# Performance work log

Measured on AMD Instinct MI355X. Metric: run time of the kernel, lower is better.

The kernel has to match this reference:

```python
import jax, jax.numpy as jnp
import numpy as np

N = 50000          # num nodes (adj_dim)
D = 128            # feature dim
E = 1_600_000      # num edges
C = 1.0            # curvature c_in
NUM_GCN_LAYERS = 3 # num_layers - 1
MIN_NORM = 1e-15
EPS = 1e-5


def hyp_logmap0(x, c):
    # Hyperboloid (Lorentz) logmap at origin, per HGCF manifold code.
    sqrtK = 1.0 / jnp.sqrt(c)            # sqrt(K), K = 1/c
    y = x[..., 1:]                        # spatial part [N, D-1]
    y_norm = jnp.maximum(jnp.linalg.norm(y, axis=-1, keepdims=True), MIN_NORM)
    theta = jnp.maximum(x[..., 0:1] / sqrtK, 1.0 + EPS)
    tail = sqrtK * jnp.arccosh(theta) * y / y_norm
    return jnp.concatenate([jnp.zeros_like(x[..., 0:1]), tail], axis=-1)


def hyp_expmap0(u, c):
    sqrtK = 1.0 / jnp.sqrt(c)
    v = u[..., 1:]
    v_norm = jnp.maximum(jnp.linalg.norm(v, axis=-1, keepdims=True), MIN_NORM)
    theta = v_norm / sqrtK
    first = sqrtK * jnp.cosh(theta)
    tail = sqrtK * jnp.sinh(theta) * v / v_norm
    return jnp.concatenate([first, tail], axis=-1)


def hyp_proj(x, c):
    # Project onto hyperboloid: reset time-like coord from spatial norm.
    K = 1.0 / c
    y = x[..., 1:]
    y_sqnorm = jnp.sum(y * y, axis=-1, keepdims=True)
    first = jnp.sqrt(jnp.maximum(K + y_sqnorm, EPS))
    return jnp.concatenate([first, y], axis=-1)


def spmm(rows, cols, vals, h):
    # sparse [N,N] @ dense [N,D] via gather + segment_sum
    return jax.ops.segment_sum(vals[:, None] * h[cols], rows, num_segments=N)


def setup_inputs() -> dict:
    key = jax.random.key(0)
    k1, k2, k3, k4 = jax.random.split(key, 4)
    # Build valid hyperboloid points: tangent vector at origin (time coord 0),
    # then expmap0 + proj.
    u_tail = 0.1 * jax.random.normal(k1, (N, D - 1), dtype=jnp.float32)
    u = jnp.concatenate([jnp.zeros((N, 1), jnp.float32), u_tail], axis=-1)
    x = hyp_proj(hyp_expmap0(u, C), C)
    adj_rows = jax.random.randint(k2, (E,), 0, N, dtype=jnp.int32)
    adj_cols = jax.random.randint(k3, (E,), 0, N, dtype=jnp.int32)
    # roughly degree-normalized positive edge weights
    adj_vals = jax.random.uniform(k4, (E,), dtype=jnp.float32) / 32.0
    return {"x": x, "adj_rows": adj_rows, "adj_cols": adj_cols, "adj_vals": adj_vals}


def reference(x, adj_rows, adj_cols, adj_vals):
    # HypAgg.forward with network='plainGCN'
    h = hyp_logmap0(x, C)
    for _ in range(NUM_GCN_LAYERS):
        h = spmm(adj_rows, adj_cols, adj_vals, h)
    out = hyp_proj(hyp_expmap0(h, C), C)
    # HyperbolicGraphConvolution returns (h, adj); adj passes through unchanged,
    # so the tensor output is `out`.
    return out
```

## Files before the change

### kernel.cpp

```cpp
#include <hip/hip_runtime.h>
#include <math.h>

#define N_NODES 50000
#define D 128
#define MIN_NORM 1e-15f
#define EPS 1e-5f
#define NBUCK 196
#define CHUNK 4096
#define CAP 9216
#define FSCALE 32.0f
#define INV_FSCALE (1.0f / 32.0f)

typedef float fx2 __attribute__((ext_vector_type(2)));

__global__ __launch_bounds__(256) void binA_kernel(const int* __restrict__ rows,
                                                   const int* __restrict__ cols,
                                                   const float* __restrict__ vals,
                                                   int* __restrict__ gcur,
                                                   int2* __restrict__ tmp, int E) {
    __shared__ int lh[NBUCK];
    __shared__ int lb[NBUCK];
    for (int i = threadIdx.x; i < NBUCK; i += 256) lh[i] = 0;
    __syncthreads();
    int start = blockIdx.x * CHUNK;
    int end = min(start + CHUNK, E);
    for (int i = start + threadIdx.x; i < end; i += 256)
        atomicAdd(&lh[rows[i] >> 8], 1);
    __syncthreads();
    for (int i = threadIdx.x; i < NBUCK; i += 256) {
        int c = lh[i];
        lb[i] = i * CAP + (c ? atomicAdd(&gcur[i], c) : 0);
        lh[i] = 0;
    }
    __syncthreads();
    for (int i = start + threadIdx.x; i < end; i += 256) {
        int r = rows[i];
        int b = r >> 8;
        int ofs = atomicAdd(&lh[b], 1);
        tmp[lb[b] + ofs] = make_int2(((r & 255) << 16) | cols[i], __float_as_int(vals[i]));
    }
}

__global__ __launch_bounds__(256) void binB_kernel(const int2* __restrict__ tmp,
                                                   const int* __restrict__ gcur,
                                                   int2* __restrict__ rowptr2,
                                                   uint2* __restrict__ epay) {
    __shared__ int hist[256];
    __shared__ int wsum[4];
    int b = blockIdx.x;
    int base = b * CAP;
    int nloc = gcur[b];
    hist[threadIdx.x] = 0;
    __syncthreads();
    for (int i = threadIdx.x; i < nloc; i += 256)
        atomicAdd(&hist[tmp[base + i].x >> 16], 1);
    __syncthreads();
    int lane = threadIdx.x & 63, wid = threadIdx.x >> 6;
    int v = hist[threadIdx.x];
    int x = v;
    #pragma unroll
    for (int off = 1; off < 64; off <<= 1) {
        int t = __shfl_up(x, off, 64);
        if (lane >= off) x += t;
    }
    if (lane == 63) wsum[wid] = x;
    __syncthreads();
    if (threadIdx.x == 0) {
        int s0 = wsum[0], s1 = wsum[1], s2 = wsum[2];
        wsum[0] = 0; wsum[1] = s0; wsum[2] = s0 + s1; wsum[3] = s0 + s1 + s2;
    }
    __syncthreads();
    int excl = x - v + wsum[wid];
    int g = (b << 8) + threadIdx.x;
    if (g < N_NODES) rowptr2[g] = make_int2(base + excl, base + excl + v);
    __syncthreads();
    hist[threadIdx.x] = excl;
    __syncthreads();
    for (int i = threadIdx.x; i < nloc; i += 256) {
        int2 p = tmp[base + i];
        int rl = p.x >> 16;
        unsigned col = (unsigned)(p.x & 0xffff);
        int pos = base + atomicAdd(&hist[rl], 1);
        epay[pos] = make_uint2(col << 7, (unsigned)p.y);
    }
}

__global__ void logmap0_kernel(const float* __restrict__ x, unsigned short* __restrict__ h) {
    int row = blockIdx.x;
    int lane = threadIdx.x;
    const float2* xr = reinterpret_cast<const float2*>(x + (size_t)row * D);
    float2 v = xr[lane];
    float x0 = __shfl(v.x, 0, 64);
    float sq = v.y * v.y + (lane == 0 ? 0.0f : v.x * v.x);
    #pragma unroll
    for (int off = 1; off < 64; off <<= 1) sq += __shfl_xor(sq, off, 64);
    float ynorm = fmaxf(sqrtf(sq), MIN_NORM);
    float theta = fmaxf(x0, 1.0f + EPS);
    float scale = FSCALE * acoshf(theta) / ynorm;
    float ox = (lane == 0) ? 0.0f : v.x * scale;
    float oy = v.y * scale;
    int packed = __builtin_amdgcn_cvt_pk_fp8_f32(ox, oy, 0, false);
    h[(size_t)row * (D / 2) + lane] = (unsigned short)packed;
}

template <bool FINAL>
__global__ __launch_bounds__(256) void spmm_kernel(const int2* __restrict__ rowptr2,
                                                   const uint2* __restrict__ epay,
                                                   const unsigned short* __restrict__ hin,
                                                   void* __restrict__ hout) {
    int lane = threadIdx.x & 63;
    int row = __builtin_amdgcn_readfirstlane(blockIdx.x * 4 + (threadIdx.x >> 6));
    int2 rp = rowptr2[row];
    int j   = __builtin_amdgcn_readfirstlane(rp.x);
    int end = __builtin_amdgcn_readfirstlane(rp.y);
    const char* hb = (const char*)hin;
    int lo = lane << 1;
    float a0 = 0.f, a1 = 0.f, b0 = 0.f, b1 = 0.f;
#define EDGE(E, A0, A1) {                                                     \
    unsigned short g8 = *(const unsigned short*)(hb + (E).x + lo);            \
    fx2 f = __builtin_amdgcn_cvt_pk_f32_fp8((int)g8, false);                  \
    float vv = __uint_as_float((E).y);                                        \
    A0 = fmaf(vv, f.x, A0); A1 = fmaf(vv, f.y, A1); }
    int t = j;
    for (; t + 8 <= end; t += 8) {
        uint2 e0 = epay[t],     e1 = epay[t + 1], e2 = epay[t + 2], e3 = epay[t + 3];
        uint2 e4 = epay[t + 4], e5 = epay[t + 5], e6 = epay[t + 6], e7 = epay[t + 7];
        EDGE(e0, a0, a1); EDGE(e1, b0, b1); EDGE(e2, a0, a1); EDGE(e3, b0, b1);
        EDGE(e4, a0, a1); EDGE(e5, b0, b1); EDGE(e6, a0, a1); EDGE(e7, b0, b1);
    }
    for (; t < end; ++t) { uint2 e = epay[t]; EDGE(e, a0, a1); }
#undef EDGE
    a0 += b0; a1 += b1;
    if (!FINAL) {
        int pk = __builtin_amdgcn_cvt_pk_fp8_f32(a0, a1, 0, false);
        ((unsigned short*)hout)[(size_t)row * (D / 2) + lane] = (unsigned short)pk;
    } else {
        a0 *= INV_FSCALE; a1 *= INV_FSCALE;
        float sq = a1 * a1 + (lane == 0 ? 0.0f : a0 * a0);
        #pragma unroll
        for (int off = 1; off < 64; off <<= 1) sq += __shfl_xor(sq, off, 64);
        float vn = fmaxf(sqrtf(sq), MIN_NORM);
        float sh = sinhf(vn);
        float scale = sh / vn;
        float first = sqrtf(fmaxf(1.0f + sh * sh, EPS));
        float2 o;
        o.x = (lane == 0) ? first : a0 * scale;
        o.y = a1 * scale;
        reinterpret_cast<float2*>((float*)hout + (size_t)row * D)[lane] = o;
    }
}

extern "C" void kernel_launch(void* const* d_in, const int* in_sizes, int n_in,
                              void* d_out, int out_size, void* d_ws, size_t ws_size,
                              hipStream_t stream) {
    const float* x    = (const float*)d_in[0];
    const int*   rows = (const int*)d_in[1];
    const int*   cols = (const int*)d_in[2];
    const float* vals = (const float*)d_in[3];
    float* out = (float*)d_out;
    int E = in_sizes[1];

    char* ws = (char*)d_ws;
    size_t REG = (size_t)NBUCK * CAP;
    int2*           tmp  = (int2*)ws;
    unsigned short* hA   = (unsigned short*)ws;
    unsigned short* hB   = (unsigned short*)(ws + (size_t)N_NODES * D);
    uint2*    epay    = (uint2*)(ws + REG * 8);
    int2*     rowptr2 = (int2*)(ws + REG * 16);
    int*      gcur    = (int*)(rowptr2 + N_NODES);

    int eb = (E + CHUNK - 1) / CHUNK;
    int sb = (N_NODES + 3) / 4;

    hipMemsetAsync(gcur, 0, NBUCK * sizeof(int), stream);
    binA_kernel<<<eb, 256, 0, stream>>>(rows, cols, vals, gcur, tmp, E);
    binB_kernel<<<NBUCK, 256, 0, stream>>>(tmp, gcur, rowptr2, epay);

    logmap0_kernel<<<N_NODES, 64, 0, stream>>>(x, hA);

    spmm_kernel<false><<<sb, 256, 0, stream>>>(rowptr2, epay, hA, hB);
    spmm_kernel<false><<<sb, 256, 0, stream>>>(rowptr2, epay, hB, hA);
    spmm_kernel<true ><<<sb, 256, 0, stream>>>(rowptr2, epay, hA, out);
}
```

Baseline: 181.7 us.

## Split SpMM into column halves with half-wave edge pairing and padded rows

Each SpMM layer now runs as two launches, each covering 64 of the 128 fp8 feature columns. Within a wave the two 32-lane halves take alternating edges, and the partial sums are combined with a cross-half shuffle. Row segments are padded to an even length with zero-weight dummy edges so edges pair cleanly, and the final expmap/proj moves into a separate epilogue kernel. The column split is meant to halve each launch's gather working set for better cache reuse, at the cost of reading the edge list twice per layer and adding launches (the memset is also replaced by a tiny kernel).

After: 329.0 us. 81.1% more time.

```diff
diff --git a/kernel.cpp b/kernel.cpp
--- a/kernel.cpp
+++ b/kernel.cpp
@@ -13,6 +13,10 @@
 
 typedef float fx2 __attribute__((ext_vector_type(2)));
 
+__global__ void zerog_kernel(int* __restrict__ gcur) {
+    if (threadIdx.x < NBUCK) gcur[threadIdx.x] = 0;
+}
+
 __global__ __launch_bounds__(256) void binA_kernel(const int* __restrict__ rows,
                                                    const int* __restrict__ cols,
                                                    const float* __restrict__ vals,
@@ -50,14 +54,16 @@
     int b = blockIdx.x;
     int base = b * CAP;
     int nloc = gcur[b];
-    hist[threadIdx.x] = 0;
-    __syncthreads();
-    for (int i = threadIdx.x; i < nloc; i += 256)
+    int tid = threadIdx.x;
+    hist[tid] = 0;
+    __syncthreads();
+    for (int i = tid; i < nloc; i += 256)
         atomicAdd(&hist[tmp[base + i].x >> 16], 1);
     __syncthreads();
-    int lane = threadIdx.x & 63, wid = threadIdx.x >> 6;
-    int v = hist[threadIdx.x];
-    int x = v;
+    int lane = tid & 63, wid = tid >> 6;
+    int v = hist[tid];
+    int r = (v + 1) & ~1;
+    int x = r;
     #pragma unroll
     for (int off = 1; off < 64; off <<= 1) {
         int t = __shfl_up(x, off, 64);
@@ -65,24 +71,25 @@
     }
     if (lane == 63) wsum[wid] = x;
     __syncthreads();
-    if (threadIdx.x == 0) {
+    if (tid == 0) {
         int s0 = wsum[0], s1 = wsum[1], s2 = wsum[2];
         wsum[0] = 0; wsum[1] = s0; wsum[2] = s0 + s1; wsum[3] = s0 + s1 + s2;
     }
     __syncthreads();
-    int excl = x - v + wsum[wid];
-    int g = (b << 8) + threadIdx.x;
-    if (g < N_NODES) rowptr2[g] = make_int2(base + excl, base + excl + v);
-    __syncthreads();
-    hist[threadIdx.x] = excl;
-    __syncthreads();
-    for (int i = threadIdx.x; i < nloc; i += 256) {
+    int excl = x - r + wsum[wid];
+    int g = (b << 8) + tid;
+    if (g < N_NODES) rowptr2[g] = make_int2(base + excl, v);
+    __syncthreads();
+    hist[tid] = excl;
+    __syncthreads();
+    for (int i = tid; i < nloc; i += 256) {
         int2 p = tmp[base + i];
         int rl = p.x >> 16;
         unsigned col = (unsigned)(p.x & 0xffff);
         int pos = base + atomicAdd(&hist[rl], 1);
         epay[pos] = make_uint2(col << 7, (unsigned)p.y);
     }
+    if (v & 1) epay[base + excl + v] = make_uint2(0u, 0u);
 }
 
 __global__ void logmap0_kernel(const float* __restrict__ x, unsigned short* __restrict__ h) {
@@ -103,51 +110,67 @@
     h[(size_t)row * (D / 2) + lane] = (unsigned short)packed;
 }
 
-template <bool FINAL>
+template <int PBASE, bool FINAL>
 __global__ __launch_bounds__(256) void spmm_kernel(const int2* __restrict__ rowptr2,
                                                    const uint2* __restrict__ epay,
-                                                   const unsigned short* __restrict__ hin,
+                                                   const unsigned char* __restrict__ hin,
                                                    void* __restrict__ hout) {
     int lane = threadIdx.x & 63;
-    int row = __builtin_amdgcn_readfirstlane(blockIdx.x * 4 + (threadIdx.x >> 6));
+    int wid = threadIdx.x >> 6;
+    int row = blockIdx.x * 4 + wid;
     int2 rp = rowptr2[row];
-    int j   = __builtin_amdgcn_readfirstlane(rp.x);
-    int end = __builtin_amdgcn_readfirstlane(rp.y);
-    const char* hb = (const char*)hin;
-    int lo = lane << 1;
+    int np = (rp.y + 1) >> 1;
+    int l32 = lane & 31;
+    const uint2* epl = epay + rp.x + (lane >> 5);
+    unsigned laneterm = (unsigned)(PBASE + (l32 << 1));
+    const unsigned char* hb = hin;
     float a0 = 0.f, a1 = 0.f, b0 = 0.f, b1 = 0.f;
-#define EDGE(E, A0, A1) {                                                     \
-    unsigned short g8 = *(const unsigned short*)(hb + (E).x + lo);            \
-    fx2 f = __builtin_amdgcn_cvt_pk_f32_fp8((int)g8, false);                  \
-    float vv = __uint_as_float((E).y);                                        \
+#define EDGE(E, A0, A1) {                                                      \
+    unsigned short g8 = *(const unsigned short*)(hb + ((E).x + laneterm));     \
+    fx2 f = __builtin_amdgcn_cvt_pk_f32_fp8((int)g8, false);                   \
+    float vv = __uint_as_float((E).y);                                         \
     A0 = fmaf(vv, f.x, A0); A1 = fmaf(vv, f.y, A1); }
-    int t = j;
-    for (; t + 8 <= end; t += 8) {
-        uint2 e0 = epay[t],     e1 = epay[t + 1], e2 = epay[t + 2], e3 = epay[t + 3];
-        uint2 e4 = epay[t + 4], e5 = epay[t + 5], e6 = epay[t + 6], e7 = epay[t + 7];
+    int t = 0;
+    for (; t + 8 <= np; t += 8) {
+        uint2 e0 = epl[2 * t],      e1 = epl[2 * t + 2],  e2 = epl[2 * t + 4],  e3 = epl[2 * t + 6];
+        uint2 e4 = epl[2 * t + 8],  e5 = epl[2 * t + 10], e6 = epl[2 * t + 12], e7 = epl[2 * t + 14];
         EDGE(e0, a0, a1); EDGE(e1, b0, b1); EDGE(e2, a0, a1); EDGE(e3, b0, b1);
         EDGE(e4, a0, a1); EDGE(e5, b0, b1); EDGE(e6, a0, a1); EDGE(e7, b0, b1);
     }
-    for (; t < end; ++t) { uint2 e = epay[t]; EDGE(e, a0, a1); }
+    for (; t < np; ++t) { uint2 e = epl[2 * t]; EDGE(e, a0, a1); }
 #undef EDGE
     a0 += b0; a1 += b1;
-    if (!FINAL) {
-        int pk = __builtin_amdgcn_cvt_pk_fp8_f32(a0, a1, 0, false);
-        ((unsigned short*)hout)[(size_t)row * (D / 2) + lane] = (unsigned short)pk;
-    } else {
-        a0 *= INV_FSCALE; a1 *= INV_FSCALE;
-        float sq = a1 * a1 + (lane == 0 ? 0.0f : a0 * a0);
-        #pragma unroll
-        for (int off = 1; off < 64; off <<= 1) sq += __shfl_xor(sq, off, 64);
-        float vn = fmaxf(sqrtf(sq), MIN_NORM);
-        float sh = sinhf(vn);
-        float scale = sh / vn;
-        float first = sqrtf(fmaxf(1.0f + sh * sh, EPS));
-        float2 o;
-        o.x = (lane == 0) ? first : a0 * scale;
-        o.y = a1 * scale;
-        reinterpret_cast<float2*>((float*)hout + (size_t)row * D)[lane] = o;
-    }
+    a0 += __shfl_xor(a0, 32, 64);
+    a1 += __shfl_xor(a1, 32, 64);
+    if (lane < 32) {
+        if (!FINAL) {
+            int pk = __builtin_amdgcn_cvt_pk_fp8_f32(a0, a1, 0, false);
+            *(unsigned short*)((unsigned char*)hout + (size_t)row * D + laneterm) =
+                (unsigned short)pk;
+        } else {
+            reinterpret_cast<float2*>((float*)hout + (size_t)row * D + PBASE)[l32] =
+                make_float2(a0, a1);
+        }
+    }
+}
+
+__global__ __launch_bounds__(256) void epilogue_kernel(float* __restrict__ out) {
+    int lane = threadIdx.x & 63;
+    int row = blockIdx.x * 4 + (threadIdx.x >> 6);
+    float2* pr = reinterpret_cast<float2*>(out + (size_t)row * D);
+    float2 v = pr[lane];
+    v.x *= INV_FSCALE; v.y *= INV_FSCALE;
+    float sq = v.y * v.y + (lane == 0 ? 0.0f : v.x * v.x);
+    #pragma unroll
+    for (int off = 1; off < 64; off <<= 1) sq += __shfl_xor(sq, off, 64);
+    float vn = fmaxf(sqrtf(sq), MIN_NORM);
+    float sh = sinhf(vn);
+    float scale = sh / vn;
+    float first = sqrtf(fmaxf(1.0f + sh * sh, EPS));
+    float2 o;
+    o.x = (lane == 0) ? first : v.x * scale;
+    o.y = v.y * scale;
+    pr[lane] = o;
 }
 
 extern "C" void kernel_launch(void* const* d_in, const int* in_sizes, int n_in,
@@ -162,9 +185,9 @@
 
     char* ws = (char*)d_ws;
     size_t REG = (size_t)NBUCK * CAP;
-    int2*           tmp  = (int2*)ws;
-    unsigned short* hA   = (unsigned short*)ws;
-    unsigned short* hB   = (unsigned short*)(ws + (size_t)N_NODES * D);
+    int2*          tmp  = (int2*)ws;
+    unsigned char* hA   = (unsigned char*)ws;
+    unsigned char* hB   = (unsigned char*)(ws + (size_t)N_NODES * D);
     uint2*    epay    = (uint2*)(ws + REG * 8);
     int2*     rowptr2 = (int2*)(ws + REG * 16);
     int*      gcur    = (int*)(rowptr2 + N_NODES);
@@ -172,13 +195,18 @@
     int eb = (E + CHUNK - 1) / CHUNK;
     int sb = (N_NODES + 3) / 4;
 
-    hipMemsetAsync(gcur, 0, NBUCK * sizeof(int), stream);
+    zerog_kernel<<<1, 256, 0, stream>>>(gcur);
     binA_kernel<<<eb, 256, 0, stream>>>(rows, cols, vals, gcur, tmp, E);
     binB_kernel<<<NBUCK, 256, 0, stream>>>(tmp, gcur, rowptr2, epay);
 
-    logmap0_kernel<<<N_NODES, 64, 0, stream>>>(x, hA);
-
-    spmm_kernel<false><<<sb, 256, 0, stream>>>(rowptr2, epay, hA, hB);
-    spmm_kernel<false><<<sb, 256, 0, stream>>>(rowptr2, epay, hB, hA);
-    spmm_kernel<true ><<<sb, 256, 0, stream>>>(rowptr2, epay, hA, out);
-}
+    logmap0_kernel<<<N_NODES, 64, 0, stream>>>(x, (unsigned short*)hA);
+
+    spmm_kernel<0,  false><<<sb, 256, 0, stream>>>(rowptr2, epay, hA, hB);
+    spmm_kernel<64, false><<<sb, 256, 0, stream>>>(rowptr2, epay, hA, hB);
+    spmm_kernel<0,  false><<<sb, 256, 0, stream>>>(rowptr2, epay, hB, hA);
+    spmm_kernel<64, false><<<sb, 256, 0, stream>>>(rowptr2, epay, hB, hA);
+    spmm_kernel<0,  true ><<<sb, 256, 0, stream>>>(rowptr2, epay, hA, out);
+    spmm_kernel<64, true ><<<sb, 256, 0, stream>>>(rowptr2, epay, hA, out);
+
+    epilogue_kernel<<<sb, 256, 0, stream>>>(out);
+}
```
